# Kernel optimization log

Hardware: AMD Instinct MI355X
Metric: run time of the kernel (lower is better)

## Reference

```python
import jax, jax.numpy as jnp
import numpy as np

B, T, C = 2, 2048, 1024
H = 16
HS = C // H  # 64
LN_EPS = 1e-5

def setup_inputs() -> dict:
    key = jax.random.key(0)
    ks = jax.random.split(key, 12)
    s = lambda *sh: 0.02
    inp = {
        'x': jax.random.normal(ks[0], (B, T, C), jnp.float32),
        # per-head Q/K/V weights (bias=False), stacked over heads: [H, C, HS]
        'wq': jax.random.normal(ks[1], (H, C, HS), jnp.float32) * 0.02,
        'wk': jax.random.normal(ks[2], (H, C, HS), jnp.float32) * 0.02,
        'wv': jax.random.normal(ks[3], (H, C, HS), jnp.float32) * 0.02,
        'w_proj': jax.random.normal(ks[4], (C, C), jnp.float32) * 0.02,
        'b_proj': jnp.zeros((C,), jnp.float32),
        'w1': jax.random.normal(ks[5], (C, 4 * C), jnp.float32) * 0.02,
        'b1': jnp.zeros((4 * C,), jnp.float32),
        'w2': jax.random.normal(ks[6], (4 * C, C), jnp.float32) * 0.02,
        'b2': jnp.zeros((C,), jnp.float32),
        'ln1_g': jnp.ones((C,), jnp.float32),
        'ln1_b': jnp.zeros((C,), jnp.float32),
        'ln2_g': jnp.ones((C,), jnp.float32),
        'ln2_b': jnp.zeros((C,), jnp.float32),
    }
    return inp

def _layernorm(x, g, b):
    mu = jnp.mean(x, axis=-1, keepdims=True)
    var = jnp.mean(jnp.square(x - mu), axis=-1, keepdims=True)
    return (x - mu) * jax.lax.rsqrt(var + LN_EPS) * g + b

def reference(x, wq, wk, wv, w_proj, b_proj, w1, b1, w2, b2, ln1_g, ln1_b, ln2_g, ln2_b):
    Bx, Tx, Cx = x.shape
    h = _layernorm(x, ln1_g, ln1_b)
    q = jnp.einsum('btc,hcd->bhtd', h, wq)
    k = jnp.einsum('btc,hcd->bhtd', h, wk)
    v = jnp.einsum('btc,hcd->bhtd', h, wv)
    # NOTE: original scales by n_embedding**-0.5 (C), not head_size**-0.5
    scores = jnp.einsum('bhtd,bhsd->bhts', q, k) * (Cx ** -0.5)
    causal = jnp.tril(jnp.ones((Tx, Tx), bool))
    scores = jnp.where(causal, scores, -jnp.inf)
    att = jax.nn.softmax(scores, axis=-1)  # [B,H,T,T]
    out = jnp.einsum('bhts,bhsd->bhtd', att, v)
    out = out.transpose(0, 2, 1, 3).reshape(Bx, Tx, Cx)  # concat heads
    out = out @ w_proj + b_proj
    x = x + out
    h2 = _layernorm(x, ln2_g, ln2_b)
    ff = jax.nn.relu(h2 @ w1 + b1) @ w2 + b2
    return x + ff
```

## Files before the change

### kernel.cpp

```cpp
#include <hip/hip_runtime.h>
#include <hip/hip_bf16.h>
#include <stdint.h>

typedef __bf16 bf16_t;
typedef __bf16 bf16x8 __attribute__((ext_vector_type(8)));
typedef __bf16 bf16x4 __attribute__((ext_vector_type(4)));
typedef float f32x4 __attribute__((ext_vector_type(4)));

static constexpr int TT = 2048, CC = 1024;

__device__ __forceinline__ void gld_lds16(const void* g, void* l) {
  __builtin_amdgcn_global_load_lds((const __attribute__((address_space(1))) void*)g,
                                   (__attribute__((address_space(3))) void*)l, 16, 0, 0);
}

__global__ __launch_bounds__(256) void transpose_all(const float* __restrict__ wq,
                                                     const float* __restrict__ wk,
                                                     const float* __restrict__ wv,
                                                     const float* __restrict__ wproj,
                                                     const float* __restrict__ w1,
                                                     const float* __restrict__ w2,
                                                     bf16_t* __restrict__ Bqkv,
                                                     bf16_t* __restrict__ Bproj,
                                                     bf16_t* __restrict__ B1w,
                                                     bf16_t* __restrict__ B2w) {
  const int id = blockIdx.x;
  const float* in;
  bf16_t* out;
  int K, N, kb, nb;
  if (id < 3072) {
    const int which = id >> 10;
    const int r = id & 1023;
    const int z = r >> 6;
    const int rr = r & 63;
    kb = rr >> 1;
    nb = rr & 1;
    K = 1024; N = 64;
    const float* srcs[3] = {wq, wk, wv};
    in = srcs[which] + (size_t)z * 1024 * 64;
    out = Bqkv + (size_t)which * 1024 * 1024 + (size_t)z * 1024 * 64;
  } else if (id < 4096) {
    const int r = id - 3072;
    kb = r >> 5; nb = r & 31;
    K = 1024; N = 1024;
    in = wproj; out = Bproj;
  } else if (id < 8192) {
    const int r = id - 4096;
    kb = r & 31; nb = r >> 5;
    K = 1024; N = 4096;
    in = w1; out = B1w;
  } else {
    const int r = id - 8192;
    kb = r >> 5; nb = r & 31;
    K = 4096; N = 1024;
    in = w2; out = B2w;
  }
  __shared__ float t[32][33];
  const int tx = threadIdx.x & 31, ty = threadIdx.x >> 5;
  const int k0 = kb * 32, n0 = nb * 32;
#pragma unroll
  for (int j = 0; j < 4; ++j)
    t[ty + j * 8][tx] = in[(size_t)(k0 + ty + j * 8) * N + n0 + tx];
  __syncthreads();
#pragma unroll
  for (int j = 0; j < 4; ++j)
    out[(size_t)(n0 + ty + j * 8) * K + k0 + tx] = (bf16_t)t[tx][ty + j * 8];
}

__global__ __launch_bounds__(256) void ln_f32_bf16(const float* __restrict__ x,
                                                   const float* __restrict__ g,
                                                   const float* __restrict__ b,
                                                   bf16_t* __restrict__ out) {
  const int row = blockIdx.x;
  const int tid = threadIdx.x;
  const float4 v = ((const float4*)(x + (size_t)row * CC))[tid];
  float s = v.x + v.y + v.z + v.w;
  float q = v.x * v.x + v.y * v.y + v.z * v.z + v.w * v.w;
#pragma unroll
  for (int off = 1; off < 64; off <<= 1) {
    s += __shfl_xor(s, off);
    q += __shfl_xor(q, off);
  }
  __shared__ float red[8];
  const int wave = tid >> 6, lane = tid & 63;
  if (lane == 0) { red[wave] = s; red[4 + wave] = q; }
  __syncthreads();
  s = red[0] + red[1] + red[2] + red[3];
  q = red[4] + red[5] + red[6] + red[7];
  const float mu = s * (1.0f / CC);
  float var = q * (1.0f / CC) - mu * mu;
  var = fmaxf(var, 0.f);
  const float rstd = rsqrtf(var + 1e-5f);
  const float4 gv = ((const float4*)g)[tid];
  const float4 bv = ((const float4*)b)[tid];
  bf16x4 o;
  o[0] = (bf16_t)((v.x - mu) * rstd * gv.x + bv.x);
  o[1] = (bf16_t)((v.y - mu) * rstd * gv.y + bv.y);
  o[2] = (bf16_t)((v.z - mu) * rstd * gv.z + bv.z);
  o[3] = (bf16_t)((v.w - mu) * rstd * gv.w + bv.w);
  *(bf16x4*)(out + (size_t)row * CC + tid * 4) = o;
}

template <int EPI, int BM, int BN, int DEPTH>
__global__ __launch_bounds__(256) void gemm_bt(const bf16_t* __restrict__ A,
                                               const bf16_t* __restrict__ Bt,
                                               void* __restrict__ Cout,
                                               const float* __restrict__ bias,
                                               const float* __restrict__ res,
                                               bf16_t* __restrict__ vt,
                                               int M, int N, int K) {
  constexpr int WM = BM / 2, WN = BN / 2;
  constexpr int MF = BM / 32, NF = BN / 32;
  constexpr int NA = BM / 32, NB = BN / 32;
  __shared__ alignas(16) bf16_t As[DEPTH][BM * 64];
  __shared__ alignas(16) bf16_t Bs[DEPTH][BN * 64];
  const int tid = threadIdx.x;
  const int wave = tid >> 6, lane = tid & 63;
  const int lr = lane & 15, lg = lane >> 4;
  const int wm = wave >> 1, wn = wave & 1;

  const int gx = gridDim.x;
  const int nwg = gx * gridDim.y;
  const int orig = (int)blockIdx.y * gx + (int)blockIdx.x;
  const int wgid = (orig & 7) * (nwg >> 3) + (orig >> 3);
  const int tm0 = (wgid / gx) * BM, tn0 = (wgid % gx) * BN;

  const int sr = lane >> 3;
  const int scs = (lane & 7) ^ sr;
  const bf16_t* Ag[NA];
#pragma unroll
  for (int i = 0; i < NA; ++i)
    Ag[i] = A + (size_t)(tm0 + i * 32 + wave * 8 + sr) * K + scs * 8;
  const bf16_t* Bg[NB];
#pragma unroll
  for (int i = 0; i < NB; ++i)
    Bg[i] = Bt + (size_t)(tn0 + i * 32 + wave * 8 + sr) * K + scs * 8;

  auto STAGE = [&](int k0, int buf) {
#pragma unroll
    for (int i = 0; i < NA; ++i)
      gld_lds16(Ag[i] + k0, &As[buf][(i * 32 + wave * 8) * 64]);
#pragma unroll
    for (int i = 0; i < NB; ++i)
      gld_lds16(Bg[i] + k0, &Bs[buf][(i * 32 + wave * 8) * 64]);
  };

  f32x4 acc[MF][NF] = {};
  const int NT = K >> 6;

  STAGE(0, 0);
  if (DEPTH == 3 && NT > 1) {
    STAGE(64, 1);
    asm volatile("s_waitcnt vmcnt(%0)" ::"i"(NA + NB) : "memory");
  } else {
    asm volatile("s_waitcnt vmcnt(0)" ::: "memory");
  }
  __builtin_amdgcn_s_barrier();

  for (int t = 0; t < NT; ++t) {
    const int cur = t % DEPTH;
    const bf16_t* Ac = As[cur];
    const bf16_t* Bc = Bs[cur];
    const bool more = (t + DEPTH - 1) < NT;
    if (more) STAGE((t + DEPTH - 1) << 6, (t + DEPTH - 1) % DEPTH);

    __builtin_amdgcn_s_setprio(1);
#pragma unroll
    for (int kk = 0; kk < 2; ++kk) {
      const int ch = ((kk * 4 + lg) ^ (lr & 7)) * 8;
      bf16x8 af[MF], bfr[NF];
#pragma unroll
      for (int n = 0; n < NF; ++n)
        bfr[n] = *(const bf16x8*)&Bc[(wn * WN + n * 16 + lr) * 64 + ch];
#pragma unroll
      for (int m = 0; m < MF; ++m)
        af[m] = *(const bf16x8*)&Ac[(wm * WM + m * 16 + lr) * 64 + ch];
#pragma unroll
      for (int m = 0; m < MF; ++m)
#pragma unroll
        for (int n = 0; n < NF; ++n)
          acc[m][n] =
              __builtin_amdgcn_mfma_f32_16x16x32_bf16(af[m], bfr[n], acc[m][n], 0, 0, 0);
    }
    __builtin_amdgcn_s_setprio(0);
    if (DEPTH == 3 && more) {
      asm volatile("s_waitcnt vmcnt(%0)" ::"i"(NA + NB) : "memory");
    } else {
      asm volatile("s_waitcnt vmcnt(0)" ::: "memory");
    }
    __builtin_amdgcn_sched_barrier(0);
    __builtin_amdgcn_s_barrier();
  }

#pragma unroll
  for (int m = 0; m < MF; ++m) {
#pragma unroll
    for (int i = 0; i < 4; ++i) {
      const int row = tm0 + wm * WM + m * 16 + lg * 4 + i;
#pragma unroll
      for (int n = 0; n < NF; ++n) {
        const int col = tn0 + wn * WN + n * 16 + lr;
        float v = acc[m][n][i];
        if (EPI == 1) v = fmaxf(v + bias[col], 0.f);
        if (EPI == 2) v = v + bias[col] + res[(size_t)row * N + col];
        if (EPI == 2) {
          ((float*)Cout)[(size_t)row * N + col] = v;
        } else if (EPI == 3) {
          if (col >= 2048) {
            const int hd = col - 2048;
            const size_t vidx =
                ((size_t)((row >> 11) * 16 + (hd >> 6)) * 64 + (hd & 63)) * TT + (row & (TT - 1));
            vt[vidx] = (bf16_t)v;
          } else {
            ((bf16_t*)Cout)[(size_t)row * N + col] = (bf16_t)v;
          }
        } else {
          ((bf16_t*)Cout)[(size_t)row * N + col] = (bf16_t)v;
        }
      }
    }
  }
}

__global__ __launch_bounds__(256, 3) void attn_fwd(const bf16_t* __restrict__ qkv,
                                                   const bf16_t* __restrict__ Vt,
                                                   bf16_t* __restrict__ O) {
  const int bh = blockIdx.x;
  const int bb = bh >> 4, hh = bh & 15;
  const int qt = 31 - (int)blockIdx.y;
  const int qbase = qt * 64;
  const int tid = threadIdx.x;
  const int wave = tid >> 6, lane = tid & 63;
  const int lr = lane & 15, lg = lane >> 4;
  const bf16_t* Qp = qkv + (size_t)bb * TT * 3072 + hh * 64;
  const bf16_t* Kp = Qp + 1024;
  const bf16_t* Vh = Vt + (size_t)bh * 64 * TT;

  constexpr int KLP = 72;
  constexpr int VLP = 136;
  constexpr int PLP = 136;
  __shared__ alignas(16) bf16_t Klds[128 * KLP];
  __shared__ alignas(16) bf16_t Vlds[64 * VLP];
  __shared__ alignas(16) bf16_t PlS[4][16 * PLP];
  bf16_t* Pw = PlS[wave];

  const int ksr = wave * 32 + (lane >> 3);
  const int ksc = (lane & 7) * 8;
  const int vsr = wave * 16 + (lane >> 4);
  const int vsc = (lane & 15) * 8;

  const int qrow = qbase + wave * 16;
  bf16x8 qf0, qf1;
  {
    const bf16x8 a = *(const bf16x8*)(Qp + (size_t)(qrow + lr) * 3072 + lg * 8);
    const bf16x8 b = *(const bf16x8*)(Qp + (size_t)(qrow + lr) * 3072 + 32 + lg * 8);
#pragma unroll
    for (int j = 0; j < 8; ++j) {
      qf0[j] = (bf16_t)((float)a[j] * 0.03125f);
      qf1[j] = (bf16_t)((float)b[j] * 0.03125f);
    }
  }

  f32x4 oacc[4] = {};
  float m_r[4], l_r[4];
#pragma unroll
  for (int i = 0; i < 4; ++i) { m_r[i] = -1e38f; l_r[i] = 0.f; }

  bf16x8 kpre[4], vpre[4];
#pragma unroll
  for (int i = 0; i < 4; ++i) {
    kpre[i] = *(const bf16x8*)(Kp + (size_t)(ksr + i * 8) * 3072 + ksc);
    vpre[i] = *(const bf16x8*)(Vh + (size_t)(vsr + i * 4) * TT + vsc);
  }
#pragma unroll
  for (int i = 0; i < 4; ++i) {
    *(bf16x8*)&Klds[(ksr + i * 8) * KLP + ksc] = kpre[i];
    *(bf16x8*)&Vlds[(vsr + i * 4) * VLP + vsc] = vpre[i];
  }
  __syncthreads();

  const int nt = (qt >> 1) + 1;
  for (int t = 0; t < nt; ++t) {
    const int s0 = t * 128;
    const int sn = (t + 1 < nt) ? s0 + 128 : s0;
#pragma unroll
    for (int i = 0; i < 4; ++i) {
      kpre[i] = *(const bf16x8*)(Kp + (size_t)(sn + ksr + i * 8) * 3072 + ksc);
      vpre[i] = *(const bf16x8*)(Vh + (size_t)(vsr + i * 4) * TT + sn + vsc);
    }

    const int u = (qrow - s0) >> 4;
    const int cmc = min(u | 1, 7);

    float P[8][4];
    __builtin_amdgcn_s_setprio(1);
#pragma unroll
    for (int ct = 0; ct < 8; ++ct) {
      if (ct <= cmc) {
        const bf16x8 kf0 = *(const bf16x8*)&Klds[(ct * 16 + lr) * KLP + lg * 8];
        const bf16x8 kf1 = *(const bf16x8*)&Klds[(ct * 16 + lr) * KLP + 32 + lg * 8];
        f32x4 z = {};
        z = __builtin_amdgcn_mfma_f32_16x16x32_bf16(qf0, kf0, z, 0, 0, 0);
        z = __builtin_amdgcn_mfma_f32_16x16x32_bf16(qf1, kf1, z, 0, 0, 0);
        if (ct >= u) {
          const int sg = s0 + ct * 16 + lr;
#pragma unroll
          for (int i = 0; i < 4; ++i)
            P[ct][i] = (sg > qrow + lg * 4 + i) ? -1e30f : z[i];
        } else {
#pragma unroll
          for (int i = 0; i < 4; ++i) P[ct][i] = z[i];
        }
      } else {
#pragma unroll
        for (int i = 0; i < 4; ++i) P[ct][i] = -1e30f;
      }
    }
    __builtin_amdgcn_s_setprio(0);

    float lmax[4];
#pragma unroll
    for (int i = 0; i < 4; ++i) {
      float m0 = fmaxf(fmaxf(P[0][i], P[1][i]), fmaxf(P[2][i], P[3][i]));
      float m1 = fmaxf(fmaxf(P[4][i], P[5][i]), fmaxf(P[6][i], P[7][i]));
      lmax[i] = fmaxf(m0, m1);
    }
    const bool ok = (lmax[0] <= m_r[0] + 8.f) && (lmax[1] <= m_r[1] + 8.f) &&
                    (lmax[2] <= m_r[2] + 8.f) && (lmax[3] <= m_r[3] + 8.f);
    if (!__all(ok)) {
      float rm[4] = {lmax[0], lmax[1], lmax[2], lmax[3]};
#pragma unroll
      for (int off = 1; off < 16; off <<= 1)
#pragma unroll
        for (int i = 0; i < 4; ++i) rm[i] = fmaxf(rm[i], __shfl_xor(rm[i], off));
#pragma unroll
      for (int i = 0; i < 4; ++i) {
        const float mn = fmaxf(m_r[i], rm[i]);
        const float alpha = __expf(m_r[i] - mn);
        m_r[i] = mn;
        l_r[i] *= alpha;
#pragma unroll
        for (int db = 0; db < 4; ++db) oacc[db][i] *= alpha;
      }
    }

#pragma unroll
    for (int i = 0; i < 4; ++i) {
      float ls = 0.f;
#pragma unroll
      for (int ct = 0; ct < 8; ++ct) {
        const float p = __expf(P[ct][i] - m_r[i]);
        P[ct][i] = p;
        ls += p;
      }
      l_r[i] += ls;
    }

#pragma unroll
    for (int ct = 0; ct < 8; ++ct) {
      if (ct <= cmc) {
#pragma unroll
        for (int i = 0; i < 4; ++i) {
          const int q = lg * 4 + i;
          const int col = (ct * 16 + lr) ^ ((lg >> 1) << 4);
          Pw[q * PLP + col] = (bf16_t)P[ct][i];
        }
      }
    }
    asm volatile("s_waitcnt lgkmcnt(0)" ::: "memory");
    __builtin_amdgcn_sched_barrier(0);

    const int kcm = cmc >> 1;
    __builtin_amdgcn_s_setprio(1);
#pragma unroll
    for (int kc = 0; kc < 4; ++kc) {
      if (kc <= kcm) {
        const bf16x8 pf =
            *(const bf16x8*)&Pw[lr * PLP + ((kc * 32 + lg * 8) ^ ((lr >> 3) << 4))];
#pragma unroll
        for (int db = 0; db < 4; ++db) {
          const bf16x8 vf = *(const bf16x8*)&Vlds[(db * 16 + lr) * VLP + kc * 32 + lg * 8];
          oacc[db] = __builtin_amdgcn_mfma_f32_16x16x32_bf16(pf, vf, oacc[db], 0, 0, 0);
        }
      }
    }
    __builtin_amdgcn_s_setprio(0);

    if (t + 1 < nt) {
      __syncthreads();
#pragma unroll
      for (int i = 0; i < 4; ++i) {
        *(bf16x8*)&Klds[(ksr + i * 8) * KLP + ksc] = kpre[i];
        *(bf16x8*)&Vlds[(vsr + i * 4) * VLP + vsc] = vpre[i];
      }
      __syncthreads();
    }
  }

#pragma unroll
  for (int off = 1; off < 16; off <<= 1)
#pragma unroll
    for (int i = 0; i < 4; ++i) l_r[i] += __shfl_xor(l_r[i], off);

  bf16_t* Op = O + ((size_t)bb * TT + qrow) * CC + hh * 64;
#pragma unroll
  for (int i = 0; i < 4; ++i) {
    const float rl = 1.0f / l_r[i];
#pragma unroll
    for (int db = 0; db < 4; ++db)
      Op[(size_t)(lg * 4 + i) * CC + db * 16 + lr] = (bf16_t)(oacc[db][i] * rl);
  }
}

extern "C" void kernel_launch(void* const* d_in, const int* in_sizes, int n_in,
                              void* d_out, int out_size, void* d_ws, size_t ws_size,
                              hipStream_t stream) {
  const float* x      = (const float*)d_in[0];
  const float* wq     = (const float*)d_in[1];
  const float* wk     = (const float*)d_in[2];
  const float* wv     = (const float*)d_in[3];
  const float* w_proj = (const float*)d_in[4];
  const float* b_proj = (const float*)d_in[5];
  const float* w1     = (const float*)d_in[6];
  const float* b1     = (const float*)d_in[7];
  const float* w2     = (const float*)d_in[8];
  const float* b2     = (const float*)d_in[9];
  const float* ln1_g  = (const float*)d_in[10];
  const float* ln1_b  = (const float*)d_in[11];
  const float* ln2_g  = (const float*)d_in[12];
  const float* ln2_b  = (const float*)d_in[13];

  char* ws = (char*)d_ws;
  const size_t MB = 1024 * 1024;
  bf16_t* h1    = (bf16_t*)(ws + 0);
  bf16_t* Bqkv  = (bf16_t*)(ws + 8 * MB);
  bf16_t* Bproj = (bf16_t*)(ws + 14 * MB);
  bf16_t* B1w   = (bf16_t*)(ws + 16 * MB);
  bf16_t* B2w   = (bf16_t*)(ws + 24 * MB);
  bf16_t* qkv   = (bf16_t*)(ws + 32 * MB);
  bf16_t* Obuf  = (bf16_t*)(ws + 56 * MB);
  float*  res1  = (float*)(ws + 64 * MB);
  bf16_t* Vt    = (bf16_t*)(ws + 64 * MB);
  bf16_t* h2    = (bf16_t*)(ws + 80 * MB);
  bf16_t* a1    = (bf16_t*)(ws + 32 * MB);
  float*  outp  = (float*)d_out;

  dim3 blk(256);
  transpose_all<<<dim3(12288), blk, 0, stream>>>(wq, wk, wv, w_proj, w1, w2,
                                                 Bqkv, Bproj, B1w, B2w);

  ln_f32_bf16<<<dim3(4096), blk, 0, stream>>>(x, ln1_g, ln1_b, h1);
  gemm_bt<3, 128, 64, 2><<<dim3(48, 32), blk, 0, stream>>>(h1, Bqkv, qkv, nullptr, nullptr,
                                                           Vt, 4096, 3072, 1024);
  attn_fwd<<<dim3(32, 32), blk, 0, stream>>>(qkv, Vt, Obuf);
  gemm_bt<2, 64, 64, 2><<<dim3(16, 64), blk, 0, stream>>>(Obuf, Bproj, res1, b_proj, x,
                                                          nullptr, 4096, 1024, 1024);
  ln_f32_bf16<<<dim3(4096), blk, 0, stream>>>(res1, ln2_g, ln2_b, h2);
  gemm_bt<1, 128, 64, 2><<<dim3(64, 32), blk, 0, stream>>>(h2, B1w, a1, b1, nullptr,
                                                           nullptr, 4096, 4096, 1024);
  gemm_bt<2, 64, 64, 2><<<dim3(16, 64), blk, 0, stream>>>(a1, B2w, outp, b2, res1,
                                                          nullptr, 4096, 1024, 4096);
}
```

Before: 246.6 us.

## Use 128x128 tiles with 8-wave workgroups for QKV and FFN1 GEMMs

Templates the GEMM on wave count so a workgroup can run 8 waves arranged 2x4, each computing a 64x32 sub-tile. The QKV and FFN-up GEMMs switch from 128x64 tiles with 256 threads to 128x128 tiles with 512 threads, which halves the grid size and raises operand reuse per byte loaded into LDS. The unused depth-3 prefetch path is removed. The trade-off is fewer workgroups per GPU (768 and 1024), which may reduce occupancy and load balance across CUs.

```diff
diff --git a/kernel.cpp b/kernel.cpp
--- a/kernel.cpp
+++ b/kernel.cpp
@@ -101,23 +101,25 @@
   *(bf16x4*)(out + (size_t)row * CC + tid * 4) = o;
 }
 
-template <int EPI, int BM, int BN, int DEPTH>
-__global__ __launch_bounds__(256) void gemm_bt(const bf16_t* __restrict__ A,
-                                               const bf16_t* __restrict__ Bt,
-                                               void* __restrict__ Cout,
-                                               const float* __restrict__ bias,
-                                               const float* __restrict__ res,
-                                               bf16_t* __restrict__ vt,
-                                               int M, int N, int K) {
-  constexpr int WM = BM / 2, WN = BN / 2;
-  constexpr int MF = BM / 32, NF = BN / 32;
-  constexpr int NA = BM / 32, NB = BN / 32;
+template <int EPI, int BM, int BN, int DEPTH, int NW>
+__global__ __launch_bounds__(NW * 64) void gemm_bt(const bf16_t* __restrict__ A,
+                                                   const bf16_t* __restrict__ Bt,
+                                                   void* __restrict__ Cout,
+                                                   const float* __restrict__ bias,
+                                                   const float* __restrict__ res,
+                                                   bf16_t* __restrict__ vt,
+                                                   int M, int N, int K) {
+  constexpr int WSN = (NW == 8) ? 4 : 2;
+  constexpr int WM = BM / 2, WN = BN / WSN;
+  constexpr int MF = WM / 16, NF = WN / 16;
+  constexpr int WROWS = NW * 8;
+  constexpr int NA = BM / WROWS, NB = BN / WROWS;
   __shared__ alignas(16) bf16_t As[DEPTH][BM * 64];
   __shared__ alignas(16) bf16_t Bs[DEPTH][BN * 64];
   const int tid = threadIdx.x;
   const int wave = tid >> 6, lane = tid & 63;
   const int lr = lane & 15, lg = lane >> 4;
-  const int wm = wave >> 1, wn = wave & 1;
+  const int wm = wave / WSN, wn = wave % WSN;
 
   const int gx = gridDim.x;
   const int nwg = gx * gridDim.y;
@@ -130,31 +132,26 @@
   const bf16_t* Ag[NA];
 #pragma unroll
   for (int i = 0; i < NA; ++i)
-    Ag[i] = A + (size_t)(tm0 + i * 32 + wave * 8 + sr) * K + scs * 8;
+    Ag[i] = A + (size_t)(tm0 + i * WROWS + wave * 8 + sr) * K + scs * 8;
   const bf16_t* Bg[NB];
 #pragma unroll
   for (int i = 0; i < NB; ++i)
-    Bg[i] = Bt + (size_t)(tn0 + i * 32 + wave * 8 + sr) * K + scs * 8;
+    Bg[i] = Bt + (size_t)(tn0 + i * WROWS + wave * 8 + sr) * K + scs * 8;
 
   auto STAGE = [&](int k0, int buf) {
 #pragma unroll
     for (int i = 0; i < NA; ++i)
-      gld_lds16(Ag[i] + k0, &As[buf][(i * 32 + wave * 8) * 64]);
+      gld_lds16(Ag[i] + k0, &As[buf][(i * WROWS + wave * 8) * 64]);
 #pragma unroll
     for (int i = 0; i < NB; ++i)
-      gld_lds16(Bg[i] + k0, &Bs[buf][(i * 32 + wave * 8) * 64]);
+      gld_lds16(Bg[i] + k0, &Bs[buf][(i * WROWS + wave * 8) * 64]);
   };
 
   f32x4 acc[MF][NF] = {};
   const int NT = K >> 6;
 
   STAGE(0, 0);
-  if (DEPTH == 3 && NT > 1) {
-    STAGE(64, 1);
-    asm volatile("s_waitcnt vmcnt(%0)" ::"i"(NA + NB) : "memory");
-  } else {
-    asm volatile("s_waitcnt vmcnt(0)" ::: "memory");
-  }
+  asm volatile("s_waitcnt vmcnt(0)" ::: "memory");
   __builtin_amdgcn_s_barrier();
 
   for (int t = 0; t < NT; ++t) {
@@ -183,11 +180,7 @@
               __builtin_amdgcn_mfma_f32_16x16x32_bf16(af[m], bfr[n], acc[m][n], 0, 0, 0);
     }
     __builtin_amdgcn_s_setprio(0);
-    if (DEPTH == 3 && more) {
-      asm volatile("s_waitcnt vmcnt(%0)" ::"i"(NA + NB) : "memory");
-    } else {
-      asm volatile("s_waitcnt vmcnt(0)" ::: "memory");
-    }
+    asm volatile("s_waitcnt vmcnt(0)" ::: "memory");
     __builtin_amdgcn_sched_barrier(0);
     __builtin_amdgcn_s_barrier();
   }
@@ -445,19 +438,19 @@
   bf16_t* a1    = (bf16_t*)(ws + 32 * MB);
   float*  outp  = (float*)d_out;
 
-  dim3 blk(256);
+  dim3 blk(256), blk512(512);
   transpose_all<<<dim3(12288), blk, 0, stream>>>(wq, wk, wv, w_proj, w1, w2,
                                                  Bqkv, Bproj, B1w, B2w);
 
   ln_f32_bf16<<<dim3(4096), blk, 0, stream>>>(x, ln1_g, ln1_b, h1);
-  gemm_bt<3, 128, 64, 2><<<dim3(48, 32), blk, 0, stream>>>(h1, Bqkv, qkv, nullptr, nullptr,
-                                                           Vt, 4096, 3072, 1024);
+  gemm_bt<3, 128, 128, 2, 8><<<dim3(24, 32), blk512, 0, stream>>>(h1, Bqkv, qkv, nullptr,
+                                                                  nullptr, Vt, 4096, 3072, 1024);
   attn_fwd<<<dim3(32, 32), blk, 0, stream>>>(qkv, Vt, Obuf);
-  gemm_bt<2, 64, 64, 2><<<dim3(16, 64), blk, 0, stream>>>(Obuf, Bproj, res1, b_proj, x,
-                                                          nullptr, 4096, 1024, 1024);
+  gemm_bt<2, 64, 64, 2, 4><<<dim3(16, 64), blk, 0, stream>>>(Obuf, Bproj, res1, b_proj, x,
+                                                             nullptr, 4096, 1024, 1024);
   ln_f32_bf16<<<dim3(4096), blk, 0, stream>>>(res1, ln2_g, ln2_b, h2);
-  gemm_bt<1, 128, 64, 2><<<dim3(64, 32), blk, 0, stream>>>(h2, B1w, a1, b1, nullptr,
-                                                           nullptr, 4096, 4096, 1024);
-  gemm_bt<2, 64, 64, 2><<<dim3(16, 64), blk, 0, stream>>>(a1, B2w, outp, b2, res1,
-                                                          nullptr, 4096, 1024, 4096);
-}
+  gemm_bt<1, 128, 128, 2, 8><<<dim3(32, 32), blk512, 0, stream>>>(h2, B1w, a1, b1, nullptr,
+                                                                  nullptr, 4096, 4096, 1024);
+  gemm_bt<2, 64, 64, 2, 4><<<dim3(16, 64), blk, 0, stream>>>(a1, B2w, outp, b2, res1,
+                                                             nullptr, 4096, 1024, 4096);
+}
```

Result: faster. 240.7 us (-2.4%).
